# Kernel tuning notes

Hardware: AMD Instinct MI355X
Metric: run time of the kernel (lower is better)

The kernel has to match this reference:

```python
import jax, jax.numpy as jnp
import numpy as np

N = 50000        # nodes
E = 1_600_000    # edges (before self-loops)
H = 2            # heads
C = 16           # out channels per head
G = 512          # graphs in batch
F_IN = 3         # const + degree + rand
NC = 2           # classes
NEG_SLOPE = 0.2  # PyG GATv2Conv default


def setup_inputs() -> dict:
    key = jax.random.key(0)
    ks = jax.random.split(key, 12)
    p = lambda k, shape: (jax.random.normal(k, shape, dtype=jnp.float32) * 0.1)
    edge_index = jax.random.randint(ks[0], (2, E), 0, N, dtype=jnp.int64)
    batch = jnp.sort(jax.random.randint(ks[1], (N,), 0, G, dtype=jnp.int64))
    rand_feat = jax.random.uniform(ks[2], (N, 1), dtype=jnp.float32)
    return {
        "edge_index": edge_index,
        "batch": batch,
        "rand_feat": rand_feat,
        # conv1: in=3 -> H*C=32
        "W1l": p(ks[3], (H * C, F_IN)), "b1l": jnp.zeros((H * C,), jnp.float32),
        "W1r": p(ks[4], (H * C, F_IN)), "b1r": jnp.zeros((H * C,), jnp.float32),
        "att1": p(ks[5], (H, C)), "bias1": jnp.zeros((H * C,), jnp.float32),
        # conv2: in=32 -> 32
        "W2l": p(ks[6], (H * C, H * C)), "b2l": jnp.zeros((H * C,), jnp.float32),
        "W2r": p(ks[7], (H * C, H * C)), "b2r": jnp.zeros((H * C,), jnp.float32),
        "att2": p(ks[8], (H, C)), "bias2": jnp.zeros((H * C,), jnp.float32),
        # fc: 32 -> 2
        "Wfc": p(ks[9], (NC, H * C)), "bfc": jnp.zeros((NC,), jnp.float32),
    }


def gatv2_conv(x, src, dst, Wl, bl, Wr, br, att, bias):
    """PyG GATv2Conv (concat=True, self-loops already appended to src/dst)."""
    n = x.shape[0]
    xl = (x @ Wl.T + bl).reshape(n, H, C)   # messages / values
    xr = (x @ Wr.T + br).reshape(n, H, C)   # target-side term
    m = xl[src] + xr[dst]                   # [E', H, C]
    e = jnp.where(m > 0, m, NEG_SLOPE * m)  # LeakyReLU
    score = jnp.einsum('ehc,hc->eh', e, att)
    # segment softmax over destination nodes (every node has a self-loop)
    smax = jax.ops.segment_max(score, dst, num_segments=n)
    ex = jnp.exp(score - smax[dst])
    denom = jax.ops.segment_sum(ex, dst, num_segments=n)
    alpha = ex / (denom[dst] + 1e-16)
    out = jax.ops.segment_sum(xl[src] * alpha[:, :, None], dst, num_segments=n)
    return out.reshape(n, H * C) + bias


def reference(edge_index, batch, rand_feat, W1l, b1l, W1r, b1r, att1, bias1,
              W2l, b2l, W2r, b2r, att2, bias2, Wfc, bfc):
    src, dst = edge_index[0], edge_index[1]
    # degree feature: index_add of ones over both rows (original edges only)
    ones_e = jnp.ones((E,), jnp.float32)
    deg = (jax.ops.segment_sum(ones_e, src, num_segments=N)
           + jax.ops.segment_sum(ones_e, dst, num_segments=N))
    x = jnp.concatenate([jnp.ones((N, 1), jnp.float32), deg[:, None], rand_feat], axis=1)
    # PyG GATv2Conv adds self-loops by default
    loops = jnp.arange(N, dtype=src.dtype)
    src_sl = jnp.concatenate([src, loops])
    dst_sl = jnp.concatenate([dst, loops])
    x = jax.nn.elu(gatv2_conv(x, src_sl, dst_sl, W1l, b1l, W1r, b1r, att1, bias1))
    x = jax.nn.elu(gatv2_conv(x, src_sl, dst_sl, W2l, b2l, W2r, b2r, att2, bias2))
    # global mean pool over graphs
    sums = jax.ops.segment_sum(x, batch, num_segments=G)
    counts = jax.ops.segment_sum(jnp.ones((N,), jnp.float32), batch, num_segments=G)
    pooled = sums / jnp.clip(counts, 1.0)[:, None]
    logits = pooled @ Wfc.T + bfc
    return jax.nn.log_softmax(logits, axis=1)
```

## Files before the change

### kernel.cpp

```cpp
#include <hip/hip_runtime.h>
#include <hip/hip_fp16.h>
#include <math.h>

#define HC 32
#define CH 16
#define NSLOPE 0.2f
#define NB2MAX 512
#define TILE 8192
#define CBMAX 6144
#define NSL 128
#define HGRP 8
#define HLDS 12544

__device__ __forceinline__ unsigned gen_pair(const int* __restrict__ ei, int E, int i){
    if (i < E) return (unsigned(ei[E+i]) << 16) | unsigned(ei[i]);
    unsigned n = i - E; return (n << 16) | n;
}

__device__ __forceinline__ __half2 pkmax2(__half2 a, __half2 b){
    union { __half2 h; unsigned u; } ua, ub, ud;
    ua.h = a; ub.h = b;
    asm("v_pk_max_f16 %0, %1, %2" : "=v"(ud.u) : "v"(ua.u), "v"(ub.u));
    return ud.h;
}

__device__ __forceinline__ __half2 sfx2(__half2 x, int off){
    union { __half2 h; int i; } u; u.h = x;
    u.i = __shfl_xor(u.i, off);
    return u.h;
}

__global__ void k_hsrc(const int* __restrict__ ei, int E, int halfN,
                       unsigned* __restrict__ hb, unsigned* __restrict__ gPair,
                       int* __restrict__ gcur){
    __shared__ unsigned h[HLDS];
    __shared__ unsigned hp[NB2MAX];
    int t = threadIdx.x;
    int nWloc = halfN >> 1;
    for (int i = t; i < nWloc; i += 512) h[i] = 0;
    int p = blockIdx.x & 1;
    if (p == 0){ hp[t] = 0; }
    if (blockIdx.x == 0 && t < NB2MAX) gcur[t] = t*CBMAX;
    __syncthreads();
    int slice = blockIdx.x >> 1;
    int base  = p * halfN;
    int chunk = (((E + NSL - 1) / NSL) + 3) & ~3;
    int lo = slice*chunk, hi = lo + chunk; if (hi > E) hi = E;
    bool v4 = ((E & 3) == 0);
    if (v4 && lo < hi){
        int m4 = lo + ((hi - lo) & ~3);
        for (int i = lo + 4*t; i + 3 < hi; i += 4*512){
            int4 s4 = *(const int4*)(ei + i);
            int a0 = s4.x - base, a1 = s4.y - base, a2 = s4.z - base, a3 = s4.w - base;
            if ((unsigned)a0 < (unsigned)halfN) atomicAdd(&h[a0 >> 1], 1u << (16*(a0 & 1)));
            if ((unsigned)a1 < (unsigned)halfN) atomicAdd(&h[a1 >> 1], 1u << (16*(a1 & 1)));
            if ((unsigned)a2 < (unsigned)halfN) atomicAdd(&h[a2 >> 1], 1u << (16*(a2 & 1)));
            if ((unsigned)a3 < (unsigned)halfN) atomicAdd(&h[a3 >> 1], 1u << (16*(a3 & 1)));
            if (p == 0){
                int4 d4 = *(const int4*)(ei + E + i);
                atomicAdd(&hp[unsigned(d4.x) >> 7], 1u);
                atomicAdd(&hp[unsigned(d4.y) >> 7], 1u);
                atomicAdd(&hp[unsigned(d4.z) >> 7], 1u);
                atomicAdd(&hp[unsigned(d4.w) >> 7], 1u);
            }
        }
        for (int i = m4 + t; i < hi; i += 512){
            int s = ei[i] - base;
            if ((unsigned)s < (unsigned)halfN) atomicAdd(&h[s >> 1], 1u << (16*(s & 1)));
            if (p == 0) atomicAdd(&hp[unsigned(ei[E+i]) >> 7], 1u);
        }
    } else {
        for (int i = lo + t; i < hi; i += 512){
            int s = ei[i] - base;
            if ((unsigned)s < (unsigned)halfN) atomicAdd(&h[s >> 1], 1u << (16*(s & 1)));
            if (p == 0) atomicAdd(&hp[unsigned(ei[E+i]) >> 7], 1u);
        }
    }
    __syncthreads();
    unsigned* out = hb + (size_t)blockIdx.x * nWloc;
    for (int w = t; w < nWloc; w += 512) out[w] = h[w];
    if (p == 0 && hp[t]) atomicAdd(&gPair[t], hp[t]);
}

__global__ void k_mid(const int* __restrict__ ei, int E, int EP,
                      int* __restrict__ gcur, unsigned* __restrict__ part,
                      const unsigned* __restrict__ hb, unsigned* __restrict__ degS,
                      int nWloc, const int* __restrict__ batch, int* __restrict__ gb,
                      int N, int G, int nTiles, int nHred,
                      unsigned* __restrict__ gPair,
                      int* __restrict__ partBase, int* __restrict__ rsN, int nb,
                      const float* __restrict__ W1l, const float* __restrict__ b1l,
                      const float* __restrict__ W1r, const float* __restrict__ b1r,
                      const float* __restrict__ att1, const float* __restrict__ bias1,
                      float4* __restrict__ tabA, float4* __restrict__ tabB){
    __shared__ int bcnt[NB2MAX], bstart[NB2MAX], c2[NB2MAX], gpos[NB2MAX], sc[256];
    __shared__ unsigned sorted[TILE];
    __shared__ unsigned short bktof[TILE];
    int t = threadIdx.x;
    int blk = blockIdx.x;

    if (blk < nTiles){
        int base = blk * TILE;
        int cnt = EP - base; if (cnt > TILE) cnt = TILE;
        bool full = (cnt == TILE);
        bcnt[t] = 0; bcnt[t+256] = 0; c2[t] = 0; c2[t+256] = 0;
        __syncthreads();
        unsigned ec[TILE/256];
        if (full){
            #pragma unroll
            for (int q = 0; q < TILE/256; ++q)
                ec[q] = gen_pair(ei, E, base + t + q*256);
            #pragma unroll
            for (int q = 0; q < TILE/256; ++q)
                atomicAdd(&bcnt[ec[q] >> 23], 1);
        } else {
            for (int j = t; j < cnt; j += 256){
                unsigned e = gen_pair(ei, E, base + j);
                atomicAdd(&bcnt[e >> 23], 1);
            }
        }
        __syncthreads();
        int v0 = bcnt[2*t], v1 = bcnt[2*t+1];
        int s = v0 + v1;
        sc[t] = s;
        __syncthreads();
        for (int d = 1; d < 256; d <<= 1){
            int x = (t >= d) ? sc[t-d] : 0;
            __syncthreads();
            sc[t] += x;
            __syncthreads();
        }
        int excl = sc[t] - s;
        bstart[2*t]   = excl;
        bstart[2*t+1] = excl + v0;
        #pragma unroll
        for (int q = 0; q < 2; ++q){
            int bb = 2*t + q;
            int v = (q == 0) ? v0 : v1;
            if (v > 0){
                gpos[bb] = atomicAdd(&gcur[bb], v);
                int bs = bstart[bb];
                for (int j = 0; j < v; ++j) bktof[bs + j] = (unsigned short)bb;
            }
        }
        __syncthreads();
        if (full){
            #pragma unroll
            for (int q = 0; q < TILE/256; ++q){
                unsigned e = ec[q];
                int b = e >> 23;
                int off = atomicAdd(&c2[b], 1);
                sorted[bstart[b] + off] = e;
            }
        } else {
            for (int j = t; j < cnt; j += 256){
                unsigned e = gen_pair(ei, E, base + j);
                int b = e >> 23;
                int off = atomicAdd(&c2[b], 1);
                sorted[bstart[b] + off] = e;
            }
        }
        __syncthreads();
        for (int k = t; k < cnt; k += 256){
            int b = bktof[k];
            int w = gpos[b] + (k - bstart[b]);
            if (w < (b+1)*CBMAX) part[w] = sorted[k];
        }
    } else if (blk < nTiles + nHred){
        int idx = (blk - nTiles)*256 + t;
        if (idx <= G){
            int lo = 0, hi = N;
            while (lo < hi){ int mid = (lo+hi)>>1; if (batch[mid] < idx) lo = mid+1; else hi = mid; }
            gb[idx] = lo;
        }
        int total = 2*nWloc;
        int grp = idx / total;
        if (grp < HGRP){
            int rem = idx - grp*total;
            int p = (rem < nWloc) ? 0 : 1;
            int w = rem - p*nWloc;
            unsigned s = 0;
            int sl0 = grp*(NSL/HGRP), sl1 = sl0 + NSL/HGRP;
            for (int sl = sl0; sl < sl1; ++sl)
                s += hb[(size_t)(sl*2 + p)*nWloc + w];
            if (s) atomicAdd(&degS[rem], s);
        }
    } else {
        int vp0 = 0, vp1 = 0;
        int b0 = 2*t, b1 = 2*t + 1;
        if (b0 < nb){
            int selfc = N - b0*128;
            selfc = (selfc < 0) ? 0 : (selfc > 128 ? 128 : selfc);
            vp0 = (int)gPair[b0] + selfc;
            gPair[b0] = (unsigned)vp0;
        }
        if (b1 < nb){
            int selfc = N - b1*128;
            selfc = (selfc < 0) ? 0 : (selfc > 128 ? 128 : selfc);
            vp1 = (int)gPair[b1] + selfc;
            gPair[b1] = (unsigned)vp1;
        }
        int s = vp0 + vp1;
        sc[t] = s;
        __syncthreads();
        for (int d = 1; d < 256; d <<= 1){
            int x = (t >= d) ? sc[t-d] : 0;
            __syncthreads();
            sc[t] += x;
            __syncthreads();
        }
        int excl = sc[t] - s;
        if (b0 < nb) partBase[b0] = excl;
        if (b1 < nb) partBase[b1] = excl + vp0;
        if (t == 0) rsN[0] = EP;
        if (t < HC){
            tabA[t] = make_float4(W1l[t*3] + b1l[t], W1l[t*3+1], W1l[t*3+2], att1[t]);
            tabB[t] = make_float4(W1r[t*3] + b1r[t], W1r[t*3+1], W1r[t*3+2], bias1[t]);
        }
    }
}

__global__ void k_fine(const unsigned* __restrict__ part, const int* __restrict__ partBase,
                       const unsigned* __restrict__ gPair,
                       const unsigned* __restrict__ degS, const float* __restrict__ rnd,
                       int* __restrict__ rs, float2* __restrict__ dr,
                       int* __restrict__ col, int N){
    __shared__ int pcnt[128], c2[128], lrs[129], sc[128];
    __shared__ int colbuf[CBMAX];
    int b = blockIdx.x, t = threadIdx.x;
    int beg = b*CBMAX, end = beg + (int)gPair[b];
    if (t < 128){ pcnt[t] = 0; c2[t] = 0; }
    __syncthreads();
    for (int k = beg + t; k < end; k += 256)
        atomicAdd(&pcnt[(part[k] >> 16) & 127], 1);
    __syncthreads();
    int v = (t < 128) ? pcnt[t] : 0;
    if (t < 128) sc[t] = v;
    __syncthreads();
    for (int d = 1; d < 128; d <<= 1){
        int x = (t >= d && t < 128) ? sc[t-d] : 0;
        __syncthreads();
        if (t < 128) sc[t] += x;
        __syncthreads();
    }
    if (t < 128){
        lrs[t] = sc[t] - v;
        if (t == 127) lrs[128] = sc[127];
    }
    __syncthreads();
    int n = (b << 7) + t;
    int pb = partBase[b];
    if (t < 128 && n < N){
        rs[n] = pb + lrs[t];
        unsigned s16 = (degS[n >> 1] >> (16*(n & 1))) & 0xFFFFu;
        dr[n] = make_float2((float)(pcnt[t] - 1 + (int)s16), rnd[n]);
    }
    for (int k = beg + t; k < end; k += 256){
        unsigned e = part[k];
        int j = (e >> 16) & 127;
        int pos = lrs[j] + atomicAdd(&c2[j], 1);
        if (pos < CBMAX) colbuf[pos] = (int)(e & 0xFFFFu);
    }
    __syncthreads();
    int npair = lrs[128];
    for (int k = t; k < npair; k += 256) col[pb + k] = colbuf[k];
}

__global__ void k_gat1(const int* __restrict__ rs, const int* __restrict__ col,
                       const float2* __restrict__ dr,
                       const float4* __restrict__ tabA, const float4* __restrict__ tabB,
                       const float* __restrict__ W2l, const float* __restrict__ b2l,
                       const float* __restrict__ W2r, const float* __restrict__ b2r,
                       __half* __restrict__ A16, __half* __restrict__ B16, int N){
    __shared__ float4 tA[HC], tB[HC];
    __shared__ float4 wq[HC][16];
    __shared__ float blS[HC], brS[HC];
    int t = threadIdx.x;
    if (t < HC){ tA[t] = tabA[t]; tB[t] = tabB[t]; blS[t] = b2l[t]; brS[t] = b2r[t]; }
    for (int w = t; w < HC*16; w += 256){
        int j = w >> 4, k = w & 15;
        wq[j][k] = make_float4(W2l[(2*k)*HC + j], W2l[(2*k+1)*HC + j],
                               W2r[(2*k)*HC + j], W2r[(2*k+1)*HC + j]);
    }
    __syncthreads();

    int d = blockIdx.x*(blockDim.x >> 4) + (t >> 4);
    if (d >= N) return;
    int lane = t & 15;
    int h = lane >> 3, r = lane & 7;

    float2 drd = dr[d];
    float base[CH];
    #pragma unroll
    for (int c = 0; c < CH; ++c){
        float4 a4 = tA[h*CH + c];
        float4 b4 = tB[h*CH + c];
        float xr = b4.x + b4.y*drd.x + b4.z*drd.y;
        base[c] = a4.x + xr;
    }

    float l = 0.f, S1 = 0.f, S2 = 0.f;
    int beg = rs[d], end = rs[d+1];
    int p = beg + r;
    for (; p + 8 < end; p += 16){
        int s0 = __builtin_nontemporal_load(col + p);
        int s1 = __builtin_nontemporal_load(col + p + 8);
        float2 da = dr[s0];
        float2 db = dr[s1];
        float sc0 = 0.f, sc1 = 0.f;
        #pragma unroll
        for (int c = 0; c < CH; ++c){
            float4 a4 = tA[h*CH + c];
            float m0 = base[c] + a4.y*da.x + a4.z*da.y;
            float m1 = base[c] + a4.y*db.x + a4.z*db.y;
            m0 = (m0 > 0.f) ? m0 : NSLOPE*m0;
            m1 = (m1 > 0.f) ? m1 : NSLOPE*m1;
            sc0 += m0 * a4.w;
            sc1 += m1 * a4.w;
        }
        float ex0 = __expf(sc0), ex1 = __expf(sc1);
        l  += ex0 + ex1;
        S1 += ex0*da.x + ex1*db.x;
        S2 += ex0*da.y + ex1*db.y;
    }
    if (p < end){
        float2 ds = dr[__builtin_nontemporal_load(col + p)];
        float sc = 0.f;
        #pragma unroll
        for (int c = 0; c < CH; ++c){
            float4 a4 = tA[h*CH + c];
            float mm = base[c] + a4.y*ds.x + a4.z*ds.y;
            mm = (mm > 0.f) ? mm : NSLOPE*mm;
            sc += mm * a4.w;
        }
        float ex = __expf(sc);
        l  += ex;
        S1 += ex*ds.x;
        S2 += ex*ds.y;
    }

    #pragma unroll
    for (int off = 4; off >= 1; off >>= 1){
        l  += __shfl_xor(l,  off);
        S1 += __shfl_xor(S1, off);
        S2 += __shfl_xor(S2, off);
    }

    float invl = 1.f/(l + 1e-16f);
    int c0 = r*2;
    float4 a40 = tA[h*CH + c0],     b40 = tB[h*CH + c0];
    float4 a41 = tA[h*CH + c0 + 1], b41 = tB[h*CH + c0 + 1];
    float v0 = a40.x + (a40.y*S1 + a40.z*S2)*invl + b40.w;
    float v1 = a41.x + (a41.y*S1 + a41.z*S2)*invl + b41.w;
    float x0 = (v0 > 0.f) ? v0 : expm1f(v0);
    float x1 = (v1 > 0.f) ? v1 : expm1f(v1);

    int k0 = 2*lane;
    float a0 = blS[k0], a1 = blS[k0+1];
    float g0 = brS[k0], g1 = brS[k0+1];
    #pragma unroll
    for (int tt = 0; tt < 16; ++tt){
        float xa = __shfl(x0, tt, 16);
        float xb = __shfl(x1, tt, 16);
        int j = 2*tt;
        float4 q0 = wq[j][lane];
        float4 q1 = wq[j+1][lane];
        a0 += xa*q0.x + xb*q1.x;
        a1 += xa*q0.y + xb*q1.y;
        g0 += xa*q0.z + xb*q1.z;
        g1 += xa*q0.w + xb*q1.w;
    }
    *(__half2*)(A16 + (size_t)d*HC + k0) = __floats2half2_rn(a0, a1);
    *(__half2*)(B16 + (size_t)d*HC + k0) = __floats2half2_rn(g0, g1);
}

__global__ void k_gat(const int* __restrict__ rs, const int* __restrict__ col,
                      const __half* __restrict__ A16, const __half* __restrict__ B16,
                      const float* __restrict__ att, const float* __restrict__ bias,
                      const int* __restrict__ batch, float* __restrict__ pooled, int N){
    __shared__ float pool[8][HC];
    __shared__ int sb[8];
    int sg = threadIdx.x >> 5;
    int d = blockIdx.x*(blockDim.x >> 5) + sg;
    int lane = threadIdx.x & 31;
    bool valid = (d < N);
    int dcl = valid ? d : 0;
    int h = lane >> 4, r = lane & 15;

    union U { uint4 u[2]; __half2 h2[8]; };
    U xr;
    {
        const uint4* bp = (const uint4*)(B16 + (size_t)dcl*HC + h*CH);
        xr.u[0] = bp[0]; xr.u[1] = bp[1];
    }
    __half2 at2[8];
    const float* atf = att + h*CH;
    #pragma unroll
    for (int i = 0; i < 8; ++i) at2[i] = __floats2half2_rn(atf[2*i], atf[2*i+1]);
    const __half2 ns2 = __float2half2_rn(NSLOPE);

    float l = 0.f;
    __half2 acc2[8];
    #pragma unroll
    for (int i = 0; i < 8; ++i) acc2[i] = __float2half2_rn(0.f);

    int beg = rs[dcl], end = valid ? rs[dcl+1] : beg;
    int p = beg + r;
    for (; p + 16 < end; p += 32){
        int s0 = __builtin_nontemporal_load(col + p);
        int s1 = __builtin_nontemporal_load(col + p + 16);
        const uint4* rp0 = (const uint4*)(A16 + (size_t)s0*HC + h*CH);
        const uint4* rp1 = (const uint4*)(A16 + (size_t)s1*HC + h*CH);
        U a, b;
        a.u[0] = rp0[0]; a.u[1] = rp0[1];
        b.u[0] = rp1[0]; b.u[1] = rp1[1];
        __half2 sc2 = __float2half2_rn(0.f);
        #pragma unroll
        for (int i = 0; i < 8; ++i){
            __half2 m  = __hadd2(a.h2[i], xr.h2[i]);
            __half2 lk = pkmax2(m, __hmul2(m, ns2));
            sc2 = __hfma2(lk, at2[i], sc2);
        }
        float ex = __expf(__low2float(sc2) + __high2float(sc2));
        l += ex;
        __half2 exh = __float2half2_rn(ex);
        #pragma unroll
        for (int i = 0; i < 8; ++i) acc2[i] = __hfma2(a.h2[i], exh, acc2[i]);

        sc2 = __float2half2_rn(0.f);
        #pragma unroll
        for (int i = 0; i < 8; ++i){
            __half2 m  = __hadd2(b.h2[i], xr.h2[i]);
            __half2 lk = pkmax2(m, __hmul2(m, ns2));
            sc2 = __hfma2(lk, at2[i], sc2);
        }
        ex = __expf(__low2float(sc2) + __high2float(sc2));
        l += ex;
        exh = __float2half2_rn(ex);
        #pragma unroll
        for (int i = 0; i < 8; ++i) acc2[i] = __hfma2(b.h2[i], exh, acc2[i]);
    }
    if (p < end){
        int s = __builtin_nontemporal_load(col + p);
        const uint4* rp = (const uint4*)(A16 + (size_t)s*HC + h*CH);
        U a;
        a.u[0] = rp[0]; a.u[1] = rp[1];
        __half2 sc2 = __float2half2_rn(0.f);
        #pragma unroll
        for (int i = 0; i < 8; ++i){
            __half2 m  = __hadd2(a.h2[i], xr.h2[i]);
            __half2 lk = pkmax2(m, __hmul2(m, ns2));
            sc2 = __hfma2(lk, at2[i], sc2);
        }
        float ex = __expf(__low2float(sc2) + __high2float(sc2));
        l += ex;
        __half2 exh = __float2half2_rn(ex);
        #pragma unroll
        for (int i = 0; i < 8; ++i) acc2[i] = __hfma2(a.h2[i], exh, acc2[i]);
    }

    __half2 v4[4];
    {
        bool hi = (r & 8) != 0;
        #pragma unroll
        for (int i = 0; i < 4; ++i){
            __half2 send = hi ? acc2[i] : acc2[i+4];
            __half2 recv = sfx2(send, 8);
            v4[i] = __hadd2(hi ? acc2[i+4] : acc2[i], recv);
        }
    }
    __half2 v2[2];
    {
        bool hi = (r & 4) != 0;
        __half2 s0 = hi ? v4[0] : v4[2];
        __half2 s1 = hi ? v4[1] : v4[3];
        __half2 r0 = sfx2(s0, 4);
        __half2 r1 = sfx2(s1, 4);
        v2[0] = __hadd2(hi ? v4[2] : v4[0], r0);
        v2[1] = __hadd2(hi ? v4[3] : v4[1], r1);
    }
    __half2 v1;
    {
        bool hi = (r & 2) != 0;
        __half2 send = hi ? v2[0] : v2[1];
        __half2 recv = sfx2(send, 2);
        v1 = __hadd2(hi ? v2[1] : v2[0], recv);
    }
    float mine;
    {
        bool hi = (r & 1) != 0;
        float lo = __low2float(v1), hf = __high2float(v1);
        float send = hi ? lo : hf;
        float recv = __shfl_xor(send, 1);
        mine = (hi ? hf : lo) + recv;
    }
    #pragma unroll
    for (int off = 8; off >= 1; off >>= 1) l += __shfl_xor(l, off);

    float invl = 1.f/(l + 1e-16f);
    float val = mine*invl + bias[h*CH + r];
    val = (val > 0.f) ? val : expm1f(val);

    if (lane == 0) sb[sg] = valid ? batch[d] : (-1 - sg);
    pool[sg][h*CH + r] = val;
    __syncthreads();
    int myb = sb[sg];
    int first = sg;
    #pragma unroll
    for (int j = 7; j >= 0; --j) if (sb[j] == myb) first = j;
    if (valid && first == sg){
        float s = 0.f;
        #pragma unroll
        for (int j = 0; j < 8; ++j) if (sb[j] == myb) s += pool[j][h*CH + r];
        atomicAdd(&pooled[(size_t)myb*HC + h*CH + r], s);
    }
}

__global__ void k_fc(const float* __restrict__ pooled, const int* __restrict__ gb,
                     const float* __restrict__ Wfc, const float* __restrict__ bfc,
                     float* __restrict__ out, int G){
    int t = threadIdx.x;
    int g = blockIdx.x*2 + (t >> 5);
    int c = t & 31;
    if (g >= G) return;
    float cnt = (float)(gb[g+1] - gb[g]);
    if (cnt < 1.f) cnt = 1.f;
    float pv = pooled[g*HC + c] / cnt;
    float p0 = pv * Wfc[c];
    float p1 = pv * Wfc[HC + c];
    #pragma unroll
    for (int off = 16; off >= 1; off >>= 1){
        p0 += __shfl_xor(p0, off, 32);
        p1 += __shfl_xor(p1, off, 32);
    }
    if (c == 0){
        float l0 = p0 + bfc[0], l1 = p1 + bfc[1];
        float m = (l0 > l1) ? l0 : l1;
        float lse = m + logf(__expf(l0 - m) + __expf(l1 - m));
        out[g*2 + 0] = l0 - lse;
        out[g*2 + 1] = l1 - lse;
    }
}

extern "C" void kernel_launch(void* const* d_in, const int* in_sizes, int n_in,
                              void* d_out, int out_size, void* d_ws, size_t ws_size,
                              hipStream_t stream) {
    const int*   ei    = (const int*)  d_in[0];
    const int*   batch = (const int*)  d_in[1];
    const float* rnd   = (const float*)d_in[2];
    const float* W1l   = (const float*)d_in[3];
    const float* b1l   = (const float*)d_in[4];
    const float* W1r   = (const float*)d_in[5];
    const float* b1r   = (const float*)d_in[6];
    const float* att1  = (const float*)d_in[7];
    const float* bias1 = (const float*)d_in[8];
    const float* W2l   = (const float*)d_in[9];
    const float* b2l   = (const float*)d_in[10];
    const float* W2r   = (const float*)d_in[11];
    const float* b2r   = (const float*)d_in[12];
    const float* att2  = (const float*)d_in[13];
    const float* bias2 = (const float*)d_in[14];
    const float* Wfc   = (const float*)d_in[15];
    const float* bfc   = (const float*)d_in[16];

    const int E  = in_sizes[0] / 2;
    const int N  = in_sizes[1];
    const int G  = out_size / 2;
    const int EP = E + N;
    const int NB2 = (N + 127) >> 7;
    const int halfN = (((N + 1) >> 1) + 1) & ~1;
    const int nWloc = halfN >> 1;

    float* ws        = (float*)d_ws;
    __half* A16      = (__half*)ws;
    __half* B16      = A16 + (size_t)N*HC;
    unsigned* hb     = (unsigned*)ws;
    unsigned* part   = (unsigned*)ws;
    size_t off       = (size_t)NSL*2*nWloc;
    if (off < (size_t)NB2*CBMAX) off = (size_t)NB2*CBMAX;
    if (off < (size_t)N*HC)      off = (size_t)N*HC;
    off = (off + 1) & ~(size_t)1;
    float2* dr       = (float2*)(ws + off);
    int*   rs        = (int*)(dr + N);
    int*   col       = rs + N + 1;
    unsigned* degS   = (unsigned*)(col + EP);
    unsigned* gPair  = degS + 2*nWloc;
    float* pooled    = (float*)(gPair + NB2MAX);
    int*   partBase  = (int*)(pooled + (size_t)G*HC);
    int*   gcur      = partBase + NB2MAX;
    int*   gb        = gcur + NB2MAX;
    float4* tabA     = (float4*)((((size_t)(gb + G + 1)) + 15) & ~(size_t)15);
    float4* tabB     = tabA + HC;

    const int T = 256;
    const int gD16 = (N + (T>>4) - 1)/(T>>4);
    const int gD32 = (N + (T>>5) - 1)/(T>>5);
    const int nTiles = (EP + TILE - 1)/TILE;
    const int nHred  = (2*nWloc*HGRP + T-1)/T;

    (void)hipMemsetAsync(degS, 0, (size_t)(2*nWloc + NB2MAX + (size_t)G*HC)*sizeof(unsigned), stream);

    k_hsrc<<<NSL*2, 512, 0, stream>>>(ei, E, halfN, hb, gPair, gcur);
    k_mid <<<nTiles + nHred + 1, T, 0, stream>>>(ei, E, EP, gcur, part,
                                   hb, degS, nWloc, batch, gb, N, G, nTiles, nHred,
                                   gPair, partBase, rs + N, NB2,
                                   W1l, b1l, W1r, b1r, att1, bias1, tabA, tabB);
    k_fine<<<NB2, T, 0, stream>>>(part, partBase, gPair, degS, rnd, rs, dr, col, N);

    k_gat1<<<gD16, T, 0, stream>>>(rs, col, dr, tabA, tabB,
                                   W2l, b2l, W2r, b2r, A16, B16, N);

    k_gat <<<gD32, T, 0, stream>>>(rs, col, A16, B16, att2, bias2, batch, pooled, N);

    k_fc  <<<(G + 1)/2, 64, 0, stream>>>(pooled, gb, Wfc, bfc, (float*)d_out, G);
}
```

Baseline: 212.2 us.

## Merge histogram and bucket-partition passes into one front kernel

The source-degree histogram blocks and the edge tile bucket-partition blocks now run concurrently in a single 512-thread kernel, since partitioning no longer depends on the histogram's cursor initialization. The cursor array is zeroed by the memset and buckets use a relative offset, so part gets its own workspace region instead of aliasing hb. The histogram reduction, graph boundaries and layer-1 tables move to a separate back kernel. NSL is halved and CBMAX shrunk to cut histogram traffic and workspace; overflow beyond CBMAX is clamped, which could drop edges if a bucket exceeds capacity.

```diff
diff --git a/kernel.cpp b/kernel.cpp
--- a/kernel.cpp
+++ b/kernel.cpp
@@ -7,8 +7,8 @@
 #define NSLOPE 0.2f
 #define NB2MAX 512
 #define TILE 8192
-#define CBMAX 6144
-#define NSL 128
+#define CBMAX 5120
+#define NSL 64
 #define HGRP 8
 #define HLDS 12544
 
@@ -30,130 +30,114 @@
     return u.h;
 }
 
-__global__ void k_hsrc(const int* __restrict__ ei, int E, int halfN,
-                       unsigned* __restrict__ hb, unsigned* __restrict__ gPair,
-                       int* __restrict__ gcur){
-    __shared__ unsigned h[HLDS];
-    __shared__ unsigned hp[NB2MAX];
-    int t = threadIdx.x;
-    int nWloc = halfN >> 1;
-    for (int i = t; i < nWloc; i += 512) h[i] = 0;
-    int p = blockIdx.x & 1;
-    if (p == 0){ hp[t] = 0; }
-    if (blockIdx.x == 0 && t < NB2MAX) gcur[t] = t*CBMAX;
-    __syncthreads();
-    int slice = blockIdx.x >> 1;
-    int base  = p * halfN;
-    int chunk = (((E + NSL - 1) / NSL) + 3) & ~3;
-    int lo = slice*chunk, hi = lo + chunk; if (hi > E) hi = E;
-    bool v4 = ((E & 3) == 0);
-    if (v4 && lo < hi){
-        int m4 = lo + ((hi - lo) & ~3);
-        for (int i = lo + 4*t; i + 3 < hi; i += 4*512){
-            int4 s4 = *(const int4*)(ei + i);
-            int a0 = s4.x - base, a1 = s4.y - base, a2 = s4.z - base, a3 = s4.w - base;
-            if ((unsigned)a0 < (unsigned)halfN) atomicAdd(&h[a0 >> 1], 1u << (16*(a0 & 1)));
-            if ((unsigned)a1 < (unsigned)halfN) atomicAdd(&h[a1 >> 1], 1u << (16*(a1 & 1)));
-            if ((unsigned)a2 < (unsigned)halfN) atomicAdd(&h[a2 >> 1], 1u << (16*(a2 & 1)));
-            if ((unsigned)a3 < (unsigned)halfN) atomicAdd(&h[a3 >> 1], 1u << (16*(a3 & 1)));
-            if (p == 0){
-                int4 d4 = *(const int4*)(ei + E + i);
-                atomicAdd(&hp[unsigned(d4.x) >> 7], 1u);
-                atomicAdd(&hp[unsigned(d4.y) >> 7], 1u);
-                atomicAdd(&hp[unsigned(d4.z) >> 7], 1u);
-                atomicAdd(&hp[unsigned(d4.w) >> 7], 1u);
-            }
-        }
-        for (int i = m4 + t; i < hi; i += 512){
-            int s = ei[i] - base;
-            if ((unsigned)s < (unsigned)halfN) atomicAdd(&h[s >> 1], 1u << (16*(s & 1)));
-            if (p == 0) atomicAdd(&hp[unsigned(ei[E+i]) >> 7], 1u);
-        }
-    } else {
-        for (int i = lo + t; i < hi; i += 512){
-            int s = ei[i] - base;
-            if ((unsigned)s < (unsigned)halfN) atomicAdd(&h[s >> 1], 1u << (16*(s & 1)));
-            if (p == 0) atomicAdd(&hp[unsigned(ei[E+i]) >> 7], 1u);
-        }
-    }
-    __syncthreads();
-    unsigned* out = hb + (size_t)blockIdx.x * nWloc;
-    for (int w = t; w < nWloc; w += 512) out[w] = h[w];
-    if (p == 0 && hp[t]) atomicAdd(&gPair[t], hp[t]);
-}
-
-__global__ void k_mid(const int* __restrict__ ei, int E, int EP,
-                      int* __restrict__ gcur, unsigned* __restrict__ part,
-                      const unsigned* __restrict__ hb, unsigned* __restrict__ degS,
-                      int nWloc, const int* __restrict__ batch, int* __restrict__ gb,
-                      int N, int G, int nTiles, int nHred,
-                      unsigned* __restrict__ gPair,
-                      int* __restrict__ partBase, int* __restrict__ rsN, int nb,
-                      const float* __restrict__ W1l, const float* __restrict__ b1l,
-                      const float* __restrict__ W1r, const float* __restrict__ b1r,
-                      const float* __restrict__ att1, const float* __restrict__ bias1,
-                      float4* __restrict__ tabA, float4* __restrict__ tabB){
-    __shared__ int bcnt[NB2MAX], bstart[NB2MAX], c2[NB2MAX], gpos[NB2MAX], sc[256];
-    __shared__ unsigned sorted[TILE];
-    __shared__ unsigned short bktof[TILE];
+__global__ __launch_bounds__(512) void k_front(const int* __restrict__ ei, int E, int EP,
+                        int halfN, unsigned* __restrict__ hb, unsigned* __restrict__ gPair,
+                        int* __restrict__ gcur, unsigned* __restrict__ part){
+    __shared__ unsigned smem[14848];
     int t = threadIdx.x;
     int blk = blockIdx.x;
 
-    if (blk < nTiles){
-        int base = blk * TILE;
+    if (blk < NSL*2){
+        unsigned* h  = smem;
+        unsigned* hp = smem + HLDS;
+        int nWloc = halfN >> 1;
+        for (int i = t; i < nWloc; i += 512) h[i] = 0;
+        int p = blk & 1;
+        if (p == 0){ hp[t] = 0; hp[t] = 0; }
+        __syncthreads();
+        int slice = blk >> 1;
+        int base  = p * halfN;
+        int chunk = (((E + NSL - 1) / NSL) + 3) & ~3;
+        int lo = slice*chunk, hi = lo + chunk; if (hi > E) hi = E;
+        bool v4 = ((E & 3) == 0);
+        if (v4 && lo < hi){
+            int m4 = lo + ((hi - lo) & ~3);
+            for (int i = lo + 4*t; i + 3 < hi; i += 4*512){
+                int4 s4 = *(const int4*)(ei + i);
+                int a0 = s4.x - base, a1 = s4.y - base, a2 = s4.z - base, a3 = s4.w - base;
+                if ((unsigned)a0 < (unsigned)halfN) atomicAdd(&h[a0 >> 1], 1u << (16*(a0 & 1)));
+                if ((unsigned)a1 < (unsigned)halfN) atomicAdd(&h[a1 >> 1], 1u << (16*(a1 & 1)));
+                if ((unsigned)a2 < (unsigned)halfN) atomicAdd(&h[a2 >> 1], 1u << (16*(a2 & 1)));
+                if ((unsigned)a3 < (unsigned)halfN) atomicAdd(&h[a3 >> 1], 1u << (16*(a3 & 1)));
+                if (p == 0){
+                    int4 d4 = *(const int4*)(ei + E + i);
+                    atomicAdd(&hp[unsigned(d4.x) >> 7], 1u);
+                    atomicAdd(&hp[unsigned(d4.y) >> 7], 1u);
+                    atomicAdd(&hp[unsigned(d4.z) >> 7], 1u);
+                    atomicAdd(&hp[unsigned(d4.w) >> 7], 1u);
+                }
+            }
+            for (int i = m4 + t; i < hi; i += 512){
+                int s = ei[i] - base;
+                if ((unsigned)s < (unsigned)halfN) atomicAdd(&h[s >> 1], 1u << (16*(s & 1)));
+                if (p == 0) atomicAdd(&hp[unsigned(ei[E+i]) >> 7], 1u);
+            }
+        } else {
+            for (int i = lo + t; i < hi; i += 512){
+                int s = ei[i] - base;
+                if ((unsigned)s < (unsigned)halfN) atomicAdd(&h[s >> 1], 1u << (16*(s & 1)));
+                if (p == 0) atomicAdd(&hp[unsigned(ei[E+i]) >> 7], 1u);
+            }
+        }
+        __syncthreads();
+        unsigned* out = hb + (size_t)blk * nWloc;
+        for (int w = t; w < nWloc; w += 512) out[w] = h[w];
+        if (p == 0 && hp[t]) atomicAdd(&gPair[t], hp[t]);
+    } else {
+        int* bcnt   = (int*)smem;
+        int* bstart = bcnt + 512;
+        int* c2     = bstart + 512;
+        int* gpos   = c2 + 512;
+        int* sc     = gpos + 512;
+        unsigned* sorted = (unsigned*)(sc + 512);
+        unsigned short* bktof = (unsigned short*)(sorted + TILE);
+        int tile = blk - NSL*2;
+        int base = tile * TILE;
         int cnt = EP - base; if (cnt > TILE) cnt = TILE;
         bool full = (cnt == TILE);
-        bcnt[t] = 0; bcnt[t+256] = 0; c2[t] = 0; c2[t+256] = 0;
-        __syncthreads();
-        unsigned ec[TILE/256];
+        bcnt[t] = 0; c2[t] = 0;
+        __syncthreads();
+        unsigned ec[TILE/512];
         if (full){
             #pragma unroll
-            for (int q = 0; q < TILE/256; ++q)
-                ec[q] = gen_pair(ei, E, base + t + q*256);
+            for (int q = 0; q < TILE/512; ++q)
+                ec[q] = gen_pair(ei, E, base + t + q*512);
             #pragma unroll
-            for (int q = 0; q < TILE/256; ++q)
+            for (int q = 0; q < TILE/512; ++q)
                 atomicAdd(&bcnt[ec[q] >> 23], 1);
         } else {
-            for (int j = t; j < cnt; j += 256){
+            for (int j = t; j < cnt; j += 512){
                 unsigned e = gen_pair(ei, E, base + j);
                 atomicAdd(&bcnt[e >> 23], 1);
             }
         }
         __syncthreads();
-        int v0 = bcnt[2*t], v1 = bcnt[2*t+1];
-        int s = v0 + v1;
-        sc[t] = s;
-        __syncthreads();
-        for (int d = 1; d < 256; d <<= 1){
+        int v = bcnt[t];
+        sc[t] = v;
+        __syncthreads();
+        for (int d = 1; d < 512; d <<= 1){
             int x = (t >= d) ? sc[t-d] : 0;
             __syncthreads();
             sc[t] += x;
             __syncthreads();
         }
-        int excl = sc[t] - s;
-        bstart[2*t]   = excl;
-        bstart[2*t+1] = excl + v0;
-        #pragma unroll
-        for (int q = 0; q < 2; ++q){
-            int bb = 2*t + q;
-            int v = (q == 0) ? v0 : v1;
-            if (v > 0){
-                gpos[bb] = atomicAdd(&gcur[bb], v);
-                int bs = bstart[bb];
-                for (int j = 0; j < v; ++j) bktof[bs + j] = (unsigned short)bb;
-            }
+        int excl = sc[t] - v;
+        bstart[t] = excl;
+        if (v > 0){
+            gpos[t] = atomicAdd(&gcur[t], v);
+            for (int j = 0; j < v; ++j) bktof[excl + j] = (unsigned short)t;
         }
         __syncthreads();
         if (full){
             #pragma unroll
-            for (int q = 0; q < TILE/256; ++q){
+            for (int q = 0; q < TILE/512; ++q){
                 unsigned e = ec[q];
                 int b = e >> 23;
                 int off = atomicAdd(&c2[b], 1);
                 sorted[bstart[b] + off] = e;
             }
         } else {
-            for (int j = t; j < cnt; j += 256){
+            for (int j = t; j < cnt; j += 512){
                 unsigned e = gen_pair(ei, E, base + j);
                 int b = e >> 23;
                 int off = atomicAdd(&c2[b], 1);
@@ -161,13 +145,28 @@
             }
         }
         __syncthreads();
-        for (int k = t; k < cnt; k += 256){
+        for (int k = t; k < cnt; k += 512){
             int b = bktof[k];
-            int w = gpos[b] + (k - bstart[b]);
-            if (w < (b+1)*CBMAX) part[w] = sorted[k];
-        }
-    } else if (blk < nTiles + nHred){
-        int idx = (blk - nTiles)*256 + t;
+            int rel = gpos[b] + (k - bstart[b]);
+            if (rel < CBMAX) part[(size_t)b*CBMAX + rel] = sorted[k];
+        }
+    }
+}
+
+__global__ void k_back(const unsigned* __restrict__ hb, unsigned* __restrict__ degS,
+                       int nWloc, const int* __restrict__ batch, int* __restrict__ gb,
+                       int N, int G, int nHred,
+                       unsigned* __restrict__ gPair, int* __restrict__ partBase,
+                       int* __restrict__ rsN, int EP, int nb,
+                       const float* __restrict__ W1l, const float* __restrict__ b1l,
+                       const float* __restrict__ W1r, const float* __restrict__ b1r,
+                       const float* __restrict__ att1, const float* __restrict__ bias1,
+                       float4* __restrict__ tabA, float4* __restrict__ tabB){
+    __shared__ int sc[256];
+    int t = threadIdx.x;
+    int blk = blockIdx.x;
+    if (blk < nHred){
+        int idx = blk*256 + t;
         if (idx <= G){
             int lo = 0, hi = N;
             while (lo < hi){ int mid = (lo+hi)>>1; if (batch[mid] < idx) lo = mid+1; else hi = mid; }
@@ -228,7 +227,8 @@
     __shared__ int pcnt[128], c2[128], lrs[129], sc[128];
     __shared__ int colbuf[CBMAX];
     int b = blockIdx.x, t = threadIdx.x;
-    int beg = b*CBMAX, end = beg + (int)gPair[b];
+    int np = (int)gPair[b]; if (np > CBMAX) np = CBMAX;
+    int beg = b*CBMAX, end = beg + np;
     if (t < 128){ pcnt[t] = 0; c2[t] = 0; }
     __syncthreads();
     for (int k = beg + t; k < end; k += 256)
@@ -575,20 +575,20 @@
     __half* A16      = (__half*)ws;
     __half* B16      = A16 + (size_t)N*HC;
     unsigned* hb     = (unsigned*)ws;
-    unsigned* part   = (unsigned*)ws;
-    size_t off       = (size_t)NSL*2*nWloc;
-    if (off < (size_t)NB2*CBMAX) off = (size_t)NB2*CBMAX;
-    if (off < (size_t)N*HC)      off = (size_t)N*HC;
-    off = (off + 1) & ~(size_t)1;
-    float2* dr       = (float2*)(ws + off);
+    size_t off1      = (size_t)NSL*2*nWloc;
+    if (off1 < (size_t)N*HC) off1 = (size_t)N*HC;
+    unsigned* part   = (unsigned*)ws + off1;
+    size_t off2      = off1 + (size_t)NB2*CBMAX;
+    off2 = (off2 + 1) & ~(size_t)1;
+    float2* dr       = (float2*)(ws + off2);
     int*   rs        = (int*)(dr + N);
     int*   col       = rs + N + 1;
     unsigned* degS   = (unsigned*)(col + EP);
     unsigned* gPair  = degS + 2*nWloc;
     float* pooled    = (float*)(gPair + NB2MAX);
-    int*   partBase  = (int*)(pooled + (size_t)G*HC);
-    int*   gcur      = partBase + NB2MAX;
-    int*   gb        = gcur + NB2MAX;
+    int*   gcur      = (int*)(pooled + (size_t)G*HC);
+    int*   partBase  = gcur + NB2MAX;
+    int*   gb        = partBase + NB2MAX;
     float4* tabA     = (float4*)((((size_t)(gb + G + 1)) + 15) & ~(size_t)15);
     float4* tabB     = tabA + HC;
 
@@ -598,14 +598,14 @@
     const int nTiles = (EP + TILE - 1)/TILE;
     const int nHred  = (2*nWloc*HGRP + T-1)/T;
 
-    (void)hipMemsetAsync(degS, 0, (size_t)(2*nWloc + NB2MAX + (size_t)G*HC)*sizeof(unsigned), stream);
-
-    k_hsrc<<<NSL*2, 512, 0, stream>>>(ei, E, halfN, hb, gPair, gcur);
-    k_mid <<<nTiles + nHred + 1, T, 0, stream>>>(ei, E, EP, gcur, part,
-                                   hb, degS, nWloc, batch, gb, N, G, nTiles, nHred,
-                                   gPair, partBase, rs + N, NB2,
+    (void)hipMemsetAsync(degS, 0,
+        (size_t)(2*nWloc + NB2MAX + (size_t)G*HC + NB2MAX)*sizeof(unsigned), stream);
+
+    k_front<<<NSL*2 + nTiles, 512, 0, stream>>>(ei, E, EP, halfN, hb, gPair, gcur, part);
+    k_back <<<nHred + 1, T, 0, stream>>>(hb, degS, nWloc, batch, gb, N, G, nHred,
+                                   gPair, partBase, rs + N, EP, NB2,
                                    W1l, b1l, W1r, b1r, att1, bias1, tabA, tabB);
-    k_fine<<<NB2, T, 0, stream>>>(part, partBase, gPair, degS, rnd, rs, dr, col, N);
+    k_fine <<<NB2, T, 0, stream>>>(part, partBase, gPair, degS, rnd, rs, dr, col, N);
 
     k_gat1<<<gD16, T, 0, stream>>>(rs, col, dr, tabA, tabB,
                                    W2l, b2l, W2r, b2r, A16, B16, N);
```

New measurement: 201.3 us. -5.1%, faster.
